# Kernel optimization log

Measured on AMD Instinct MI355X. Metric: run time of the kernel, lower is better.

The kernel has to match this reference:

```python
import jax, jax.numpy as jnp
import numpy as np

C = 4096      # n_channels (total blocks)
B = 2048      # active blocks (len(indices))
T = 1024      # coords per block
DIN, DH, DOUT = 3, 64, 3
OMEGA0 = 30.0


def setup_inputs() -> dict:
    key = jax.random.key(0)
    ks = jax.random.split(key, 12)
    inp = jax.random.normal(ks[0], (C, T, DIN), dtype=jnp.float32)
    indices = jax.random.randint(ks[1], (B,), 0, C)
    # SIREN init: first layer uniform(-1/in, 1/in); hidden uniform(-sqrt(6/in)/w0, ...)
    b_first = 1.0 / DIN
    b_hid = float(np.sqrt(6.0 / DH) / OMEGA0)
    b_last = float(np.sqrt(1.0 / DH) / OMEGA0)
    u = lambda k, shape, b: jax.random.uniform(k, shape, jnp.float32, -b, b)
    return {
        "inp": inp, "indices": indices,
        "W0": u(ks[2], (C, DIN, DH), b_first), "b0": u(ks[3], (C, 1, DH), b_first),
        "W1": u(ks[4], (C, DH, DH), b_hid),   "b1": u(ks[5], (C, 1, DH), b_hid),
        "W2": u(ks[6], (C, DH, DH), b_hid),   "b2": u(ks[7], (C, 1, DH), b_hid),
        "W3": u(ks[8], (C, DH, DOUT), b_last), "b3": u(ks[9], (C, 1, DOUT), b_last),
    }


def _adaptive_linear(x, W, b, idx):
    # gather per-active-block weights then batched matmul: [B,T,i] @ [B,i,o] + [B,1,o]
    return jnp.einsum('bti,bio->bto', x, W[idx]) + b[idx]


def reference(inp, indices, W0, b0, W1, b1, W2, b2, W3, b3):
    x = inp[indices]                                     # [B,T,DIN]
    x = jnp.sin(OMEGA0 * _adaptive_linear(x, W0, b0, indices))
    x = jnp.sin(OMEGA0 * _adaptive_linear(x, W1, b1, indices))
    x = jnp.sin(OMEGA0 * _adaptive_linear(x, W2, b2, indices))
    x = _adaptive_linear(x, W3, b3, indices)             # outermost linear
    return x                                             # [B,T,DOUT]
```

## Files before the change

kernel.cpp:

```cpp
#include <hip/hip_runtime.h>
#include <hip/hip_bf16.h>


namespace {

constexpr int   TPTS = 1024;
constexpr float C30  = 30.0f * 0.15915494309189535f;

typedef float        f32x4 __attribute__((ext_vector_type(4)));
typedef short        s16x8 __attribute__((ext_vector_type(8)));
typedef unsigned int u32x4 __attribute__((ext_vector_type(4)));
typedef unsigned int u32x2 __attribute__((ext_vector_type(2)));

__device__ __forceinline__ unsigned short bfr(float x) {
    __hip_bfloat16 h = __float2bfloat16(x);
    unsigned short u;
    __builtin_memcpy(&u, &h, sizeof(u));
    return u;
}
__device__ __forceinline__ float bf2f(unsigned short u) {
    unsigned int w = (unsigned int)u << 16;
    float f;
    __builtin_memcpy(&f, &w, sizeof(f));
    return f;
}
__device__ __forceinline__ float sin_rev(float r) {
    return __builtin_amdgcn_sinf(__builtin_amdgcn_fractf(r));
}

__device__ __forceinline__ void act_store(const f32x4 (&acc)[4][2],
                                          unsigned char* lh,
                                          int tw, int l15, int kg) {
    const unsigned swz = (unsigned)(l15 & 7) << 4;
    #pragma unroll
    for (int ni = 0; ni < 4; ++ni) {
        #pragma unroll
        for (int tj = 0; tj < 2; ++tj) {
            f32x4 a = acc[ni][tj];
            unsigned short s0 = bfr(sin_rev(a[0]));
            unsigned short s1 = bfr(sin_rev(a[1]));
            unsigned short s2 = bfr(sin_rev(a[2]));
            unsigned short s3 = bfr(sin_rev(a[3]));
            u32x2 p;
            p[0] = (unsigned)s0 | ((unsigned)s1 << 16);
            p[1] = (unsigned)s2 | ((unsigned)s3 << 16);
            const int trow = tw + tj * 16 + l15;
            *(u32x2*)(lh + trow * 128 +
                      (((unsigned)(ni * 32 + kg * 8)) ^ swz)) = p;
        }
    }
}

__device__ __forceinline__ void hidden_layer(f32x4 (&acc)[4][2],
                                             const s16x8 (&wf)[2][4],
                                             const unsigned char* lh,
                                             const float* lb,
                                             int tw, int l15, int kg) {
    const unsigned swz = (unsigned)(l15 & 7) << 4;
    #pragma unroll
    for (int ni = 0; ni < 4; ++ni) {
        f32x4 bv = *(const f32x4*)(lb + ni * 16 + kg * 4);
        #pragma unroll
        for (int tj = 0; tj < 2; ++tj) acc[ni][tj] = bv;
    }
    #pragma unroll
    for (int ks = 0; ks < 2; ++ks) {
        const unsigned ko = (unsigned)(ks * 64 + kg * 16);
        s16x8 hf[2];
        #pragma unroll
        for (int tj = 0; tj < 2; ++tj)
            hf[tj] = *(const s16x8*)(lh + (tw + tj * 16 + l15) * 128 + (ko ^ swz));
        #pragma unroll
        for (int ni = 0; ni < 4; ++ni) {
            #pragma unroll
            for (int tj = 0; tj < 2; ++tj)
                acc[ni][tj] = __builtin_amdgcn_mfma_f32_16x16x32_bf16(
                    wf[ks][ni], hf[tj], acc[ni][tj], 0, 0, 0);
        }
    }
}

}

__global__ __launch_bounds__(256, 4) void siren_fused(
    const float* __restrict__ inp, const int* __restrict__ indices,
    const float* __restrict__ W0, const float* __restrict__ b0,
    const float* __restrict__ W1, const float* __restrict__ b1,
    const float* __restrict__ W2, const float* __restrict__ b2,
    const float* __restrict__ W3, const float* __restrict__ b3,
    float* __restrict__ out)
{
    __shared__ __align__(16) unsigned char lds[37376];
    unsigned char* const lh  = lds;
    unsigned char* const lw1 = lds + 16384;
    unsigned char* const lw2 = lds + 24576;
    unsigned char* const lw3 = lds + 32768;
    unsigned char* const lw0 = lds + 34816;
    float*         const lbias = (float*)(lds + 36864);

    const int tid  = threadIdx.x;
    const int lane = tid & 63;
    const int wid  = tid >> 6;
    const int l15  = lane & 15;
    const int kg   = lane >> 4;
    const int bid  = blockIdx.x;

    const int idx = __builtin_amdgcn_readfirstlane(indices[bid]);

    const float* const W0g = W0 + (size_t)idx * 192;
    const float* const b0g = b0 + (size_t)idx * 64;
    const float* const W1g = W1 + (size_t)idx * 4096;
    const float* const b1g = b1 + (size_t)idx * 64;
    const float* const W2g = W2 + (size_t)idx * 4096;
    const float* const b2g = b2 + (size_t)idx * 64;
    const float* const W3g = W3 + (size_t)idx * 192;
    const float* const b3g = b3 + (size_t)idx * 3;

    {
        const int n  = tid & 63;
        const int kc = (tid >> 6) * 16;
        const unsigned rowb = (unsigned)n * 128u;
        const unsigned swzn = (unsigned)(n & 7) << 4;
        #pragma unroll
        for (int w = 0; w < 2; ++w) {
            const float* Wg = w ? W2g : W1g;
            unsigned char* lw = w ? lw2 : lw1;
            unsigned int q[8];
            #pragma unroll
            for (int j = 0; j < 8; ++j) {
                unsigned short e0 = bfr(Wg[(kc + 2 * j    ) * 64 + n] * C30);
                unsigned short e1 = bfr(Wg[(kc + 2 * j + 1) * 64 + n] * C30);
                q[j] = (unsigned)e0 | ((unsigned)e1 << 16);
            }
            u32x4 q0 = {q[0], q[1], q[2], q[3]};
            u32x4 q1 = {q[4], q[5], q[6], q[7]};
            *(u32x4*)(lw + rowb + (((unsigned)(kc * 2)      ) ^ swzn)) = q0;
            *(u32x4*)(lw + rowb + (((unsigned)(kc * 2) + 16u) ^ swzn)) = q1;
        }
        if (tid < 128) {
            const int g = tid >> 6, o = tid & 63;
            const float* bg = g ? b2g : b1g;
            lbias[tid] = bg[o] * C30;
        }
        if (tid < 208) {
            u32x2 z; z[0] = 0u; z[1] = 0u;
            *(u32x2*)(lw3 + 384 + tid * 8) = z;
        }
        if (tid < 64) {
            const int k = tid;
            #pragma unroll
            for (int c = 0; c < 3; ++c) {
                unsigned short v = bfr(W3g[k * 3 + c]);
                *(unsigned short*)(lw3 + (unsigned)c * 128u +
                                   (((unsigned)(2 * k)) ^ ((unsigned)c << 4))) = v;
            }
            unsigned short wh[3], wl[3];
            #pragma unroll
            for (int i = 0; i < 3; ++i) {
                float ws = W0g[i * 64 + k] * C30;
                wh[i] = bfr(ws);
                wl[i] = bfr(ws - bf2f(wh[i]));
            }
            const float bs = b0g[k] * C30;
            unsigned short Bhi = bfr(bs);
            unsigned short Blo = bfr(bs - bf2f(Bhi));
            u32x4 r0 = { (unsigned)wh[0] | ((unsigned)wh[1] << 16),
                         (unsigned)wh[2] | ((unsigned)Bhi   << 16),
                         (unsigned)wh[0] | ((unsigned)wh[1] << 16),
                         (unsigned)wh[2] | ((unsigned)Blo   << 16) };
            u32x4 r1 = { (unsigned)wl[0] | ((unsigned)wl[1] << 16),
                         (unsigned)wl[2], 0u, 0u };
            *(u32x4*)(lw0 + k * 32)      = r0;
            *(u32x4*)(lw0 + k * 32 + 16) = r1;
        }
    }
    __syncthreads();

    const unsigned swz = (unsigned)(l15 & 7) << 4;

    s16x8 w1r[2][4], w2r[2][4];
    #pragma unroll
    for (int ks = 0; ks < 2; ++ks) {
        const unsigned ko = (unsigned)(ks * 64 + kg * 16);
        #pragma unroll
        for (int ni = 0; ni < 4; ++ni) {
            w1r[ks][ni] = *(const s16x8*)(lw1 + (ni * 16 + l15) * 128 + (ko ^ swz));
            w2r[ks][ni] = *(const s16x8*)(lw2 + (ni * 16 + l15) * 128 + (ko ^ swz));
        }
    }

    const float* const xg = inp + (size_t)idx * (TPTS * 3);
    float*       const og = out + (size_t)bid * (TPTS * 3);
    const int tw = wid * 32;

    #pragma unroll 1
    for (int tile = 0; tile < 8; ++tile) {
        const int tbase = tile * 128 + tw;

        s16x8 xf[2];
        #pragma unroll
        for (int tj = 0; tj < 2; ++tj) {
            const float* xr = xg + (size_t)(tbase + tj * 16 + l15) * 3;
            float x0 = xr[0], x1 = xr[1], x2 = xr[2];
            unsigned short h0 = bfr(x0), h1 = bfr(x1), h2 = bfr(x2);
            unsigned short g0 = bfr(x0 - bf2f(h0));
            unsigned short g1 = bfr(x1 - bf2f(h1));
            unsigned short g2 = bfr(x2 - bf2f(h2));
            const bool hi = (kg < 2), lo = (kg == 0);
            const short one = lo ? (short)0x3F80 : (short)0;
            s16x8 v;
            v[0] = hi ? (short)h0 : (short)0;
            v[1] = hi ? (short)h1 : (short)0;
            v[2] = hi ? (short)h2 : (short)0;
            v[3] = one;
            v[4] = lo ? (short)g0 : (short)0;
            v[5] = lo ? (short)g1 : (short)0;
            v[6] = lo ? (short)g2 : (short)0;
            v[7] = one;
            xf[tj] = v;
        }
        f32x4 acc[4][2];
        #pragma unroll
        for (int ni = 0; ni < 4; ++ni) {
            #pragma unroll
            for (int tj = 0; tj < 2; ++tj) {
                f32x4 z; z[0] = 0.f; z[1] = 0.f; z[2] = 0.f; z[3] = 0.f;
                acc[ni][tj] = z;
            }
        }
        #pragma unroll
        for (int ni = 0; ni < 4; ++ni) {
            const s16x8 wf = *(const s16x8*)(lw0 + (ni * 16 + l15) * 32 + (kg & 1) * 16);
            #pragma unroll
            for (int tj = 0; tj < 2; ++tj)
                acc[ni][tj] = __builtin_amdgcn_mfma_f32_16x16x32_bf16(
                    wf, xf[tj], acc[ni][tj], 0, 0, 0);
        }
        act_store(acc, lh, tw, l15, kg);

        hidden_layer(acc, w1r, lh, lbias,      tw, l15, kg);
        act_store(acc, lh, tw, l15, kg);
        hidden_layer(acc, w2r, lh, lbias + 64, tw, l15, kg);
        act_store(acc, lh, tw, l15, kg);

        {
            const float bb0 = b3g[0], bb1 = b3g[1], bb2 = b3g[2];
            f32x4 acc3[2];
            #pragma unroll
            for (int tj = 0; tj < 2; ++tj) {
                f32x4 c; c[0] = bb0; c[1] = bb1; c[2] = bb2; c[3] = 0.0f;
                acc3[tj] = c;
            }
            #pragma unroll
            for (int ks = 0; ks < 2; ++ks) {
                const unsigned ko = (unsigned)(ks * 64 + kg * 16);
                const s16x8 wf = *(const s16x8*)(lw3 + l15 * 128 + (ko ^ swz));
                #pragma unroll
                for (int tj = 0; tj < 2; ++tj) {
                    const s16x8 hf = *(const s16x8*)(lh + (tw + tj * 16 + l15) * 128 + (ko ^ swz));
                    acc3[tj] = __builtin_amdgcn_mfma_f32_16x16x32_bf16(
                        wf, hf, acc3[tj], 0, 0, 0);
                }
            }
            if (kg == 0) {
                #pragma unroll
                for (int tj = 0; tj < 2; ++tj) {
                    float* o = og + (size_t)(tbase + tj * 16 + l15) * 3;
                    o[0] = acc3[tj][0];
                    o[1] = acc3[tj][1];
                    o[2] = acc3[tj][2];
                }
            }
        }
    }
}

extern "C" void kernel_launch(void* const* d_in, const int* in_sizes, int n_in,
                              void* d_out, int out_size, void* d_ws, size_t ws_size,
                              hipStream_t stream) {
    (void)in_sizes; (void)n_in; (void)out_size; (void)d_ws; (void)ws_size;
    siren_fused<<<dim3(2048), dim3(256), 0, stream>>>(
        (const float*)d_in[0], (const int*)d_in[1],
        (const float*)d_in[2], (const float*)d_in[3],
        (const float*)d_in[4], (const float*)d_in[5],
        (const float*)d_in[6], (const float*)d_in[7],
        (const float*)d_in[8], (const float*)d_in[9],
        (float*)d_out);
}
```

Baseline: 248.1 us.

## Alias weight staging into activation LDS buffer and prefetch next tile inputs

The W1/W2 staging area now reuses the activation buffer region, since the weights are copied into registers before the main loop starts. This cuts LDS use per block from about 37KB to 21KB so more blocks can be resident per CU, at the cost of an extra barrier. Input coordinates for the next tile are loaded one iteration ahead into registers to hide global load latency. The W0 LDS layout is also split into two planes so fragment reads are contiguous.

New measurement: 248.7 us. No clear change (+0.2%).

```diff
diff --git a/kernel.cpp b/kernel.cpp
--- a/kernel.cpp
+++ b/kernel.cpp
@@ -90,13 +90,11 @@
     const float* __restrict__ W3, const float* __restrict__ b3,
     float* __restrict__ out)
 {
-    __shared__ __align__(16) unsigned char lds[37376];
+    __shared__ __align__(16) unsigned char lds[20992];
     unsigned char* const lh  = lds;
-    unsigned char* const lw1 = lds + 16384;
-    unsigned char* const lw2 = lds + 24576;
-    unsigned char* const lw3 = lds + 32768;
-    unsigned char* const lw0 = lds + 34816;
-    float*         const lbias = (float*)(lds + 36864);
+    unsigned char* const lw3 = lds + 16384;
+    unsigned char* const lw0 = lds + 18432;
+    float*         const lbias = (float*)(lds + 20480);
 
     const int tid  = threadIdx.x;
     const int lane = tid & 63;
@@ -124,7 +122,7 @@
         #pragma unroll
         for (int w = 0; w < 2; ++w) {
             const float* Wg = w ? W2g : W1g;
-            unsigned char* lw = w ? lw2 : lw1;
+            unsigned char* lw = lh + (w ? 8192 : 0);
             unsigned int q[8];
             #pragma unroll
             for (int j = 0; j < 8; ++j) {
@@ -170,8 +168,8 @@
                          (unsigned)wh[2] | ((unsigned)Blo   << 16) };
             u32x4 r1 = { (unsigned)wl[0] | ((unsigned)wl[1] << 16),
                          (unsigned)wl[2], 0u, 0u };
-            *(u32x4*)(lw0 + k * 32)      = r0;
-            *(u32x4*)(lw0 + k * 32 + 16) = r1;
+            *(u32x4*)(lw0 + k * 16)        = r0;
+            *(u32x4*)(lw0 + 1024 + k * 16) = r1;
         }
     }
     __syncthreads();
@@ -184,15 +182,24 @@
         const unsigned ko = (unsigned)(ks * 64 + kg * 16);
         #pragma unroll
         for (int ni = 0; ni < 4; ++ni) {
-            w1r[ks][ni] = *(const s16x8*)(lw1 + (ni * 16 + l15) * 128 + (ko ^ swz));
-            w2r[ks][ni] = *(const s16x8*)(lw2 + (ni * 16 + l15) * 128 + (ko ^ swz));
-        }
-    }
+            w1r[ks][ni] = *(const s16x8*)(lh        + (ni * 16 + l15) * 128 + (ko ^ swz));
+            w2r[ks][ni] = *(const s16x8*)(lh + 8192 + (ni * 16 + l15) * 128 + (ko ^ swz));
+        }
+    }
+    __syncthreads();
 
     const float* const xg = inp + (size_t)idx * (TPTS * 3);
     float*       const og = out + (size_t)bid * (TPTS * 3);
     const int tw = wid * 32;
 
+    float xa[3], xb[3];
+    {
+        const float* r0 = xg + (size_t)(tw      + l15) * 3;
+        const float* r1 = xg + (size_t)(tw + 16 + l15) * 3;
+        xa[0] = r0[0]; xa[1] = r0[1]; xa[2] = r0[2];
+        xb[0] = r1[0]; xb[1] = r1[1]; xb[2] = r1[2];
+    }
+
     #pragma unroll 1
     for (int tile = 0; tile < 8; ++tile) {
         const int tbase = tile * 128 + tw;
@@ -200,8 +207,8 @@
         s16x8 xf[2];
         #pragma unroll
         for (int tj = 0; tj < 2; ++tj) {
-            const float* xr = xg + (size_t)(tbase + tj * 16 + l15) * 3;
-            float x0 = xr[0], x1 = xr[1], x2 = xr[2];
+            const float* xs = tj ? xb : xa;
+            float x0 = xs[0], x1 = xs[1], x2 = xs[2];
             unsigned short h0 = bfr(x0), h1 = bfr(x1), h2 = bfr(x2);
             unsigned short g0 = bfr(x0 - bf2f(h0));
             unsigned short g1 = bfr(x1 - bf2f(h1));
@@ -219,6 +226,16 @@
             v[7] = one;
             xf[tj] = v;
         }
+        {
+            const int nb = (tile < 7) ? tbase + 128 : tbase;
+            const float* r0 = xg + (size_t)(nb      + l15) * 3;
+            const float* r1 = xg + (size_t)(nb + 16 + l15) * 3;
+            float n0 = r0[0], n1 = r0[1], n2 = r0[2];
+            float n3 = r1[0], n4 = r1[1], n5 = r1[2];
+            xa[0] = n0; xa[1] = n1; xa[2] = n2;
+            xb[0] = n3; xb[1] = n4; xb[2] = n5;
+        }
+
         f32x4 acc[4][2];
         #pragma unroll
         for (int ni = 0; ni < 4; ++ni) {
@@ -230,7 +247,7 @@
         }
         #pragma unroll
         for (int ni = 0; ni < 4; ++ni) {
-            const s16x8 wf = *(const s16x8*)(lw0 + (ni * 16 + l15) * 32 + (kg & 1) * 16);
+            const s16x8 wf = *(const s16x8*)(lw0 + (kg & 1) * 1024 + (ni * 16 + l15) * 16);
             #pragma unroll
             for (int tj = 0; tj < 2; ++tj)
                 acc[ni][tj] = __builtin_amdgcn_mfma_f32_16x16x32_bf16(
```
